# Kernel tuning notes

Hardware: AMD Instinct MI355X
Metric: run time of the kernel (lower is better)

Reference implementation:

```python
import jax, jax.numpy as jnp
import numpy as np

N = 50000        # nodes
E = 800000       # edges (no self loops; GATv2Conv adds them itself)
F_IN = 256       # n_feats
DIM_H = 64       # hidden per head (layer 1)
HEADS = 4        # heads (layer 1)
N_CLASSES = 10
NEG_SLOPE = 0.2


def setup_inputs() -> dict:
    key = jax.random.key(0)
    ks = jax.random.split(key, 12)
    x = jax.random.normal(ks[0], (N, F_IN), dtype=jnp.float32)
    # edges with src != dst so PyG's remove_self_loops is a no-op
    src = jax.random.randint(ks[1], (E,), 0, N, dtype=jnp.int32)
    off = jax.random.randint(ks[2], (E,), 1, N, dtype=jnp.int32)
    dst = (src + off) % N
    edge_index = jnp.stack([src, dst], axis=0)  # [2, E]
    HC = HEADS * DIM_H
    s1 = 1.0 / np.sqrt(F_IN)
    s2 = 1.0 / np.sqrt(HC)
    W_l1 = jax.random.normal(ks[3], (F_IN, HC), dtype=jnp.float32) * s1
    W_r1 = jax.random.normal(ks[4], (F_IN, HC), dtype=jnp.float32) * s1
    att1 = jax.random.normal(ks[5], (HEADS, DIM_H), dtype=jnp.float32) * s2
    b1 = jnp.zeros((HC,), dtype=jnp.float32)
    W_l2 = jax.random.normal(ks[6], (HC, N_CLASSES), dtype=jnp.float32) * s2
    W_r2 = jax.random.normal(ks[7], (HC, N_CLASSES), dtype=jnp.float32) * s2
    att2 = jax.random.normal(ks[8], (1, N_CLASSES), dtype=jnp.float32) * (1.0 / np.sqrt(N_CLASSES))
    b2 = jnp.zeros((N_CLASSES,), dtype=jnp.float32)
    return {"x": x, "edge_index": edge_index,
            "W_l1": W_l1, "W_r1": W_r1, "att1": att1, "b1": b1,
            "W_l2": W_l2, "W_r2": W_r2, "att2": att2, "b2": b2}


def _gatv2_layer(x, src, dst, W_l, W_r, att, b, heads, ch):
    """One GATv2Conv layer (concat heads). src/dst already include self loops."""
    n = x.shape[0]
    xl = (x @ W_l).reshape(n, heads, ch)  # source transform (messages)
    xr = (x @ W_r).reshape(n, heads, ch)  # target transform
    # per-edge GATv2 score: att . LeakyReLU(x_l[src] + x_r[dst])
    e = jax.nn.leaky_relu(xl[src] + xr[dst], NEG_SLOPE)   # [E, H, C]
    score = jnp.einsum('ehc,hc->eh', e, att)              # [E, H]
    # segment softmax over incoming edges of each dst node
    m = jax.ops.segment_max(score, dst, num_segments=n)   # [N, H]
    ex = jnp.exp(score - m[dst])
    denom = jax.ops.segment_sum(ex, dst, num_segments=n)  # [N, H]
    alpha = ex / denom[dst]                               # [E, H]
    msg = xl[src] * alpha[:, :, None]                     # [E, H, C]
    out = jax.ops.segment_sum(msg, dst, num_segments=n)   # [N, H, C]
    return out.reshape(n, heads * ch) + b


def reference(x, edge_index, W_l1, W_r1, att1, b1, W_l2, W_r2, att2, b2):
    n = x.shape[0]
    loops = jnp.arange(n, dtype=edge_index.dtype)
    src = jnp.concatenate([edge_index[0], loops])  # add_self_loops=True
    dst = jnp.concatenate([edge_index[1], loops])
    h = _gatv2_layer(x, src, dst, W_l1, W_r1, att1, b1, HEADS, DIM_H)
    h = jax.nn.relu(h)
    out = _gatv2_layer(h, src, dst, W_l2, W_r2, att2, b2, 1, N_CLASSES)
    return out
```

## Files before the change

kernel.cpp:

```cpp
#include <hip/hip_runtime.h>
#include <hip/hip_bf16.h>

typedef unsigned short u16;
typedef unsigned int u32;
typedef short bf16x8 __attribute__((ext_vector_type(8)));
typedef float f32x4 __attribute__((ext_vector_type(4)));

constexpr int N_NODES = 50000;
constexpr int N_EDGES = 800000;
constexpr int ET      = N_EDGES + N_NODES;
constexpr int HC      = 256;
constexpr int NCLS    = 10;
constexpr float NEG   = 0.2f;

__device__ __forceinline__ u16 f2bf(float f) {
  u32 u = __float_as_uint(f);
  u += 0x7fffu + ((u >> 16) & 1u);
  return (u16)(u >> 16);
}
__device__ __forceinline__ float bf2f(u16 h) {
  return __uint_as_float(((u32)h) << 16);
}

__device__ __forceinline__ float dpp_ror8(float v) {
  return __uint_as_float(__builtin_amdgcn_mov_dpp(__float_as_uint(v), 0x128, 0xf, 0xf, true));
}
__device__ __forceinline__ float dpp_ror4(float v) {
  return __uint_as_float(__builtin_amdgcn_mov_dpp(__float_as_uint(v), 0x124, 0xf, 0xf, true));
}
__device__ __forceinline__ float dpp_ror2(float v) {
  return __uint_as_float(__builtin_amdgcn_mov_dpp(__float_as_uint(v), 0x122, 0xf, 0xf, true));
}
__device__ __forceinline__ float dpp_ror1(float v) {
  return __uint_as_float(__builtin_amdgcn_mov_dpp(__float_as_uint(v), 0x121, 0xf, 0xf, true));
}
__device__ __forceinline__ float row16_allsum(float p) {
  p += dpp_ror8(p);
  p += dpp_ror4(p);
  p += dpp_ror2(p);
  p += dpp_ror1(p);
  return p;
}


__global__ void k_zero_int(int* __restrict__ p, int n) {
  int i = blockIdx.x * 256 + threadIdx.x;
  if (i < n) p[i] = 0;
}

__global__ void k_hist(const int* __restrict__ ei, int* __restrict__ counts) {
  int e = blockIdx.x * 256 + threadIdx.x;
  if (e >= ET) return;
  int d = (e < N_EDGES) ? ei[N_EDGES + e] : (e - N_EDGES);
  atomicAdd(&counts[d], 1);
}

__global__ __launch_bounds__(256) void k_scan1(const int* __restrict__ counts,
                                               int* __restrict__ offsets,
                                               int* __restrict__ bsums) {
  __shared__ int sd[256];
  int t = threadIdx.x;
  int base = blockIdx.x * 1024 + t * 4;
  int v[4];
#pragma unroll
  for (int i = 0; i < 4; ++i) {
    int idx = base + i;
    v[i] = (idx < N_NODES) ? counts[idx] : 0;
  }
  int tsum = v[0] + v[1] + v[2] + v[3];
  sd[t] = tsum;
  __syncthreads();
  for (int off = 1; off < 256; off <<= 1) {
    int x = (t >= off) ? sd[t - off] : 0;
    __syncthreads();
    sd[t] += x;
    __syncthreads();
  }
  int run = sd[t] - tsum;
#pragma unroll
  for (int i = 0; i < 4; ++i) {
    run += v[i];
    int idx = base + i;
    if (idx < N_NODES) offsets[idx + 1] = run;
  }
  if (t == 255) bsums[blockIdx.x] = sd[255];
}

__global__ __launch_bounds__(256) void k_scan2(int* __restrict__ bsums, int nb) {
  __shared__ int sd[256];
  int t = threadIdx.x;
  int v = (t < nb) ? bsums[t] : 0;
  sd[t] = v;
  __syncthreads();
  for (int off = 1; off < 256; off <<= 1) {
    int x = (t >= off) ? sd[t - off] : 0;
    __syncthreads();
    sd[t] += x;
    __syncthreads();
  }
  if (t < nb) bsums[t] = sd[t] - v;
}

__global__ void k_scan3(const int* __restrict__ bsums, int* __restrict__ offsets) {
  int i = blockIdx.x * 256 + threadIdx.x;
  if (i < N_NODES) offsets[i + 1] += bsums[i >> 10];
  if (i == 0) offsets[0] = 0;
}

__global__ void k_scatter(const int* __restrict__ ei, const int* __restrict__ offsets,
                          int* __restrict__ counts, int* __restrict__ srcs) {
  int e = blockIdx.x * 256 + threadIdx.x;
  if (e >= ET) return;
  int s, d;
  if (e < N_EDGES) { s = ei[e]; d = ei[N_EDGES + e]; }
  else             { s = e - N_EDGES; d = s; }
  int pos = offsets[d] + atomicSub(&counts[d], 1) - 1;
  srcs[pos] = s;
}

__global__ __launch_bounds__(256) void k_packW(const float* __restrict__ Wl,
                                               const float* __restrict__ Wr,
                                               u16* __restrict__ Wt_hi,
                                               u16* __restrict__ Wt_lo) {
  int c = blockIdx.x;
  int k = threadIdx.x;
  float w = (c < 256) ? Wl[k * 256 + c] : Wr[k * 256 + (c - 256)];
  u16 h = f2bf(w);
  float lo = w - bf2f(h);
  Wt_hi[c * 256 + k] = h;
  Wt_lo[c * 256 + k] = f2bf(lo);
}

__global__ __launch_bounds__(256) void k_gemm1_mfma(const float* __restrict__ x,
                                                    const u16* __restrict__ Wt_hi,
                                                    const u16* __restrict__ Wt_lo,
                                                    float* __restrict__ xl,
                                                    float* __restrict__ xr) {
  __shared__ char smem[61440];
  char* Ah = smem;
  char* Al = smem + 10240;
  char* Bh = smem + 20480;
  char* Bl = smem + 40960;

  int t = threadIdx.x;
  int lane = t & 63, wave = t >> 6;
  int wm = wave >> 1, wn = wave & 1;
  int row0 = blockIdx.x * 128;
  int bc = blockIdx.y;
  int col0 = bc * 256;

  f32x4 acc[4][8];
#pragma unroll
  for (int m = 0; m < 4; ++m)
#pragma unroll
    for (int n = 0; n < 8; ++n) acc[m][n] = (f32x4){0.f, 0.f, 0.f, 0.f};

  int ar = t >> 3;
  int ak4 = t & 7;
  int rr = lane & 15, kb = lane >> 4;

#pragma unroll 1
  for (int kk = 0; kk < 256; kk += 32) {
#pragma unroll
    for (int i = 0; i < 4; ++i) {
      int r = ar + 32 * i;
      int grow = row0 + r;
      if (grow >= N_NODES) grow = N_NODES - 1;
      float4 v = *(const float4*)&x[(size_t)grow * 256 + kk + ak4 * 4];
      u16 h0 = f2bf(v.x), h1 = f2bf(v.y), h2 = f2bf(v.z), h3 = f2bf(v.w);
      u16 l0 = f2bf(v.x - bf2f(h0)), l1 = f2bf(v.y - bf2f(h1));
      u16 l2 = f2bf(v.z - bf2f(h2)), l3 = f2bf(v.w - bf2f(h3));
      uint2 hp = make_uint2((u32)h0 | ((u32)h1 << 16), (u32)h2 | ((u32)h3 << 16));
      uint2 lp = make_uint2((u32)l0 | ((u32)l1 << 16), (u32)l2 | ((u32)l3 << 16));
      int boff = r * 80 + ak4 * 8;
      *(uint2*)(Ah + boff) = hp;
      *(uint2*)(Al + boff) = lp;
    }
    {
      const u16* sh = &Wt_hi[(size_t)(col0 + t) * 256 + kk];
      const u16* sl = &Wt_lo[(size_t)(col0 + t) * 256 + kk];
#pragma unroll
      for (int j = 0; j < 4; ++j) {
        *(uint4*)(Bh + t * 80 + j * 16) = *(const uint4*)&sh[j * 8];
        *(uint4*)(Bl + t * 80 + j * 16) = *(const uint4*)&sl[j * 8];
      }
    }
    __syncthreads();
    bf16x8 a_h[4], a_l[4];
#pragma unroll
    for (int m = 0; m < 4; ++m) {
      int off = (wm * 64 + m * 16 + rr) * 80 + kb * 16;
      a_h[m] = *(const bf16x8*)(Ah + off);
      a_l[m] = *(const bf16x8*)(Al + off);
    }
#pragma unroll
    for (int n = 0; n < 8; ++n) {
      int off = (wn * 128 + n * 16 + rr) * 80 + kb * 16;
      bf16x8 b_h = *(const bf16x8*)(Bh + off);
      bf16x8 b_l = *(const bf16x8*)(Bl + off);
#pragma unroll
      for (int m = 0; m < 4; ++m) {
        acc[m][n] = __builtin_amdgcn_mfma_f32_16x16x32_bf16(a_h[m], b_h, acc[m][n], 0, 0, 0);
        acc[m][n] = __builtin_amdgcn_mfma_f32_16x16x32_bf16(a_l[m], b_h, acc[m][n], 0, 0, 0);
        acc[m][n] = __builtin_amdgcn_mfma_f32_16x16x32_bf16(a_h[m], b_l, acc[m][n], 0, 0, 0);
      }
    }
    __syncthreads();
  }
  float* Cout = bc ? xr : xl;
  int r0w = row0 + wm * 64 + (lane >> 4) * 4;
  int c0w = wn * 128 + (lane & 15);
#pragma unroll
  for (int m = 0; m < 4; ++m)
#pragma unroll
    for (int j = 0; j < 4; ++j) {
      int grow = r0w + m * 16 + j;
      if (grow < N_NODES) {
#pragma unroll
        for (int n = 0; n < 8; ++n)
          Cout[(size_t)grow * 256 + c0w + n * 16] = acc[m][n][j];
      }
    }
}

__global__ __launch_bounds__(256) void k_gat1_fused(
    const float* __restrict__ xl, const float* __restrict__ xr,
    const float* __restrict__ att, const float* __restrict__ b1,
    const float* __restrict__ Wl2, const float* __restrict__ Wr2,
    const int* __restrict__ offsets, const int* __restrict__ srcs,
    float* __restrict__ xl2, float* __restrict__ xr2) {
  __shared__ float Ws[20][256];
  int t = threadIdx.x;
#pragma unroll
  for (int c = 0; c < 10; ++c) {
    Ws[c][t]      = Wl2[t * 10 + c];
    Ws[c + 10][t] = Wr2[t * 10 + c];
  }
  __syncthreads();

  int wave = t >> 6, lane = t & 63;
  int n = blockIdx.x * 4 + wave;
  int c0 = lane * 4;
  float4 attv = *(const float4*)&att[c0];
  float4 xrv  = *(const float4*)&xr[(size_t)n * 256 + c0];

  float m0 = -1e30f, m1 = -1e30f, m2 = -1e30f, m3 = -1e30f;
  float d0 = 0.f, d1 = 0.f, d2 = 0.f, d3 = 0.f;
  float4 A0 = {0,0,0,0}, A1 = {0,0,0,0}, A2 = {0,0,0,0}, A3 = {0,0,0,0};

  auto proc = [&](float4 xv, float& m, float& d, float4& A) {
    float e0 = xv.x + xrv.x; e0 = fmaxf(e0, NEG * e0);
    float e1 = xv.y + xrv.y; e1 = fmaxf(e1, NEG * e1);
    float e2 = xv.z + xrv.z; e2 = fmaxf(e2, NEG * e2);
    float e3 = xv.w + xrv.w; e3 = fmaxf(e3, NEG * e3);
    float p = attv.x * e0 + attv.y * e1 + attv.z * e2 + attv.w * e3;
    p = row16_allsum(p);
    float mn = fmaxf(m, p);
    float corr = __expf(m - mn);
    float w    = __expf(p - mn);
    d = d * corr + w;
    A.x = A.x * corr + w * xv.x;
    A.y = A.y * corr + w * xv.y;
    A.z = A.z * corr + w * xv.z;
    A.w = A.w * corr + w * xv.w;
    m = mn;
  };

  int jb = offsets[n], je = offsets[n + 1];
  int j = jb;
  for (; j + 4 <= je; j += 4) {
    int s0 = srcs[j], s1 = srcs[j + 1], s2 = srcs[j + 2], s3 = srcs[j + 3];
    float4 x0 = *(const float4*)&xl[(size_t)s0 * 256 + c0];
    float4 x1 = *(const float4*)&xl[(size_t)s1 * 256 + c0];
    float4 x2 = *(const float4*)&xl[(size_t)s2 * 256 + c0];
    float4 x3 = *(const float4*)&xl[(size_t)s3 * 256 + c0];
    proc(x0, m0, d0, A0);
    proc(x1, m1, d1, A1);
    proc(x2, m2, d2, A2);
    proc(x3, m3, d3, A3);
  }
  for (; j < je; ++j) {
    int s = srcs[j];
    float4 xv = *(const float4*)&xl[(size_t)s * 256 + c0];
    proc(xv, m0, d0, A0);
  }

  auto merge = [](float& ma, float& da, float4& Aa, float mb, float db, float4 Ab) {
    float mm = fmaxf(ma, mb);
    float fa = __expf(ma - mm), fb = __expf(mb - mm);
    da = da * fa + db * fb;
    Aa.x = Aa.x * fa + Ab.x * fb;
    Aa.y = Aa.y * fa + Ab.y * fb;
    Aa.z = Aa.z * fa + Ab.z * fb;
    Aa.w = Aa.w * fa + Ab.w * fb;
    ma = mm;
  };
  merge(m0, d0, A0, m1, d1, A1);
  merge(m2, d2, A2, m3, d3, A3);
  merge(m0, d0, A0, m2, d2, A2);

  float inv = 1.0f / d0;
  float4 bv = *(const float4*)&b1[c0];
  float4 ov;
  ov.x = fmaxf(A0.x * inv + bv.x, 0.f);
  ov.y = fmaxf(A0.y * inv + bv.y, 0.f);
  ov.z = fmaxf(A0.z * inv + bv.z, 0.f);
  ov.w = fmaxf(A0.w * inv + bv.w, 0.f);

  float p[20];
#pragma unroll
  for (int c = 0; c < 20; ++c) {
    float4 w4 = *(const float4*)&Ws[c][c0];
    p[c] = ov.x * w4.x + ov.y * w4.y + ov.z * w4.z + ov.w * w4.w;
  }
#pragma unroll
  for (int c = 0; c < 20; ++c) {
    p[c] = row16_allsum(p[c]);
    p[c] += __shfl_xor(p[c], 16);
    p[c] += __shfl_xor(p[c], 32);
  }
  if (lane == 0) {
#pragma unroll
    for (int c = 0; c < 10; ++c) xl2[n * NCLS + c] = p[c];
#pragma unroll
    for (int c = 0; c < 10; ++c) xr2[n * NCLS + c] = p[c + 10];
  }
}

__global__ __launch_bounds__(256) void k_gat2(const float* __restrict__ xl2,
                                              const float* __restrict__ xr2,
                                              const float* __restrict__ att2,
                                              const float* __restrict__ b2,
                                              const int* __restrict__ offsets,
                                              const int* __restrict__ srcs,
                                              float* __restrict__ out) {
  int wave = threadIdx.x >> 6;
  int lane = threadIdx.x & 63;
  int n = blockIdx.x * 4 + wave;
  if (n >= N_NODES) return;
  int g = lane >> 4;
  int k = lane & 15;
  bool act = k < NCLS;
  float attk = act ? att2[k] : 0.f;
  float xrk  = act ? xr2[n * NCLS + k] : 0.f;
  float m = -1e30f;
  float denom = 0.f, acc = 0.f;
  int jb = offsets[n], je = offsets[n + 1];
  for (int j = jb + g; j < je; j += 4) {
    int s = srcs[j];
    float xlv = act ? xl2[s * NCLS + k] : 0.f;
    float e = xlv + xrk; e = fmaxf(e, NEG * e);
    float p = attk * e;
    p = row16_allsum(p);
    float mn = fmaxf(m, p);
    float corr = __expf(m - mn);
    float w    = __expf(p - mn);
    denom = denom * corr + w;
    acc   = acc * corr + w * xlv;
    m = mn;
  }
  float mg = fmaxf(m, __shfl_xor(m, 16));
  mg = fmaxf(mg, __shfl_xor(mg, 32));
  float f = __expf(m - mg);
  float d = denom * f;
  d += __shfl_xor(d, 16);
  d += __shfl_xor(d, 32);
  float a = acc * f;
  a += __shfl_xor(a, 16);
  a += __shfl_xor(a, 32);
  if (act && g == 0) out[n * NCLS + k] = a / d + b2[k];
}


extern "C" void kernel_launch(void* const* d_in, const int* in_sizes, int n_in,
                              void* d_out, int out_size, void* d_ws, size_t ws_size,
                              hipStream_t stream) {
  const float* x    = (const float*)d_in[0];
  const int*   ei   = (const int*)d_in[1];
  const float* Wl1  = (const float*)d_in[2];
  const float* Wr1  = (const float*)d_in[3];
  const float* att1 = (const float*)d_in[4];
  const float* b1   = (const float*)d_in[5];
  const float* Wl2  = (const float*)d_in[6];
  const float* Wr2  = (const float*)d_in[7];
  const float* att2 = (const float*)d_in[8];
  const float* b2   = (const float*)d_in[9];
  float* out = (float*)d_out;

  int* offsets = (int*)d_ws;
  int* counts  = offsets + (N_NODES + 1);
  int* bsums   = counts + N_NODES;
  int* srcs    = bsums + 256;
  size_t int_count = (size_t)(N_NODES + 1) + N_NODES + 256 + ET;
  size_t foff = (int_count + 63) & ~(size_t)63;
  float* xl1 = (float*)d_ws + foff;
  float* xr1 = xl1 + (size_t)N_NODES * HC;
  u16* Wt_hi = (u16*)(xr1 + (size_t)N_NODES * HC);
  u16* Wt_lo = Wt_hi + 512 * 256;
  float* xl2 = (float*)(Wt_lo + 512 * 256);
  float* xr2 = xl2 + (size_t)N_NODES * NCLS;

  const int nthr = 256;
  k_zero_int<<<(N_NODES + nthr - 1) / nthr, nthr, 0, stream>>>(counts, N_NODES);
  k_hist<<<(ET + nthr - 1) / nthr, nthr, 0, stream>>>(ei, counts);
  int nb = (N_NODES + 1023) / 1024;
  k_scan1<<<nb, nthr, 0, stream>>>(counts, offsets, bsums);
  k_scan2<<<1, nthr, 0, stream>>>(bsums, nb);
  k_scan3<<<(N_NODES + nthr - 1) / nthr, nthr, 0, stream>>>(bsums, offsets);
  k_scatter<<<(ET + nthr - 1) / nthr, nthr, 0, stream>>>(ei, offsets, counts, srcs);

  k_packW<<<512, nthr, 0, stream>>>(Wl1, Wr1, Wt_hi, Wt_lo);
  dim3 g1((N_NODES + 127) / 128, 2);
  k_gemm1_mfma<<<g1, nthr, 0, stream>>>(x, Wt_hi, Wt_lo, xl1, xr1);

  k_gat1_fused<<<N_NODES / 4, nthr, 0, stream>>>(xl1, xr1, att1, b1, Wl2, Wr2,
                                                 offsets, srcs, xl2, xr2);

  k_gat2<<<(N_NODES + 3) / 4, nthr, 0, stream>>>(xl2, xr2, att2, b2, offsets, srcs, out);
}
```

Before: 424.0 us.

## Store layer-1 features in bf16, pad CSR rows, use lazy exp2 softmax rescaling

The GEMM now writes xl/xr as bf16 instead of fp32, which halves the bytes gathered per edge in the layer-1 aggregation. CSR segments are padded to multiples of four with -1 sentinels, so the remainder loop goes away. Online softmax now uses exp2 with log2e folded into att and skips rescaling unless the max grows by more than a threshold. The zero kernel becomes a memset. The cost is bf16 rounding error in the layer-1 features and extra memset traffic for the padded index array.

```diff
diff --git a/kernel.cpp b/kernel.cpp
--- a/kernel.cpp
+++ b/kernel.cpp
@@ -9,9 +9,11 @@
 constexpr int N_NODES = 50000;
 constexpr int N_EDGES = 800000;
 constexpr int ET      = N_EDGES + N_NODES;
+constexpr int ETP     = ET + 3 * N_NODES;
 constexpr int HC      = 256;
 constexpr int NCLS    = 10;
 constexpr float NEG   = 0.2f;
+constexpr float LOG2E = 1.442695041f;
 
 __device__ __forceinline__ u16 f2bf(float f) {
   u32 u = __float_as_uint(f);
@@ -42,11 +44,6 @@
   return p;
 }
 
-
-__global__ void k_zero_int(int* __restrict__ p, int n) {
-  int i = blockIdx.x * 256 + threadIdx.x;
-  if (i < n) p[i] = 0;
-}
 
 __global__ void k_hist(const int* __restrict__ ei, int* __restrict__ counts) {
   int e = blockIdx.x * 256 + threadIdx.x;
@@ -65,7 +62,7 @@
 #pragma unroll
   for (int i = 0; i < 4; ++i) {
     int idx = base + i;
-    v[i] = (idx < N_NODES) ? counts[idx] : 0;
+    v[i] = (idx < N_NODES) ? ((counts[idx] + 3) & ~3) : 0;
   }
   int tsum = v[0] + v[1] + v[2] + v[3];
   sd[t] = tsum;
@@ -134,8 +131,8 @@
 __global__ __launch_bounds__(256) void k_gemm1_mfma(const float* __restrict__ x,
                                                     const u16* __restrict__ Wt_hi,
                                                     const u16* __restrict__ Wt_lo,
-                                                    float* __restrict__ xl,
-                                                    float* __restrict__ xr) {
+                                                    u16* __restrict__ xlb,
+                                                    u16* __restrict__ xrb) {
   __shared__ char smem[61440];
   char* Ah = smem;
   char* Al = smem + 10240;
@@ -207,7 +204,7 @@
     }
     __syncthreads();
   }
-  float* Cout = bc ? xr : xl;
+  u16* Cout = bc ? xrb : xlb;
   int r0w = row0 + wm * 64 + (lane >> 4) * 4;
   int c0w = wn * 128 + (lane & 15);
 #pragma unroll
@@ -218,13 +215,13 @@
       if (grow < N_NODES) {
 #pragma unroll
         for (int n = 0; n < 8; ++n)
-          Cout[(size_t)grow * 256 + c0w + n * 16] = acc[m][n][j];
+          Cout[(size_t)grow * 256 + c0w + n * 16] = f2bf(acc[m][n][j]);
       }
     }
 }
 
 __global__ __launch_bounds__(256) void k_gat1_fused(
-    const float* __restrict__ xl, const float* __restrict__ xr,
+    const u16* __restrict__ xlb, const u16* __restrict__ xrb,
     const float* __restrict__ att, const float* __restrict__ b1,
     const float* __restrict__ Wl2, const float* __restrict__ Wr2,
     const int* __restrict__ offsets, const int* __restrict__ srcs,
@@ -242,52 +239,49 @@
   int n = blockIdx.x * 4 + wave;
   int c0 = lane * 4;
   float4 attv = *(const float4*)&att[c0];
-  float4 xrv  = *(const float4*)&xr[(size_t)n * 256 + c0];
+  attv.x *= LOG2E; attv.y *= LOG2E; attv.z *= LOG2E; attv.w *= LOG2E;
+  ushort4 xr4 = *(const ushort4*)&xrb[(size_t)n * 256 + c0];
+  float4 xrv = make_float4(bf2f(xr4.x), bf2f(xr4.y), bf2f(xr4.z), bf2f(xr4.w));
 
   float m0 = -1e30f, m1 = -1e30f, m2 = -1e30f, m3 = -1e30f;
   float d0 = 0.f, d1 = 0.f, d2 = 0.f, d3 = 0.f;
   float4 A0 = {0,0,0,0}, A1 = {0,0,0,0}, A2 = {0,0,0,0}, A3 = {0,0,0,0};
 
-  auto proc = [&](float4 xv, float& m, float& d, float4& A) {
+  auto proc = [&](int s, float& m, float& d, float4& A) {
+    int sa = s < 0 ? 0 : s;
+    ushort4 r4 = *(const ushort4*)&xlb[(size_t)sa * 256 + c0];
+    float4 xv = make_float4(bf2f(r4.x), bf2f(r4.y), bf2f(r4.z), bf2f(r4.w));
     float e0 = xv.x + xrv.x; e0 = fmaxf(e0, NEG * e0);
     float e1 = xv.y + xrv.y; e1 = fmaxf(e1, NEG * e1);
     float e2 = xv.z + xrv.z; e2 = fmaxf(e2, NEG * e2);
     float e3 = xv.w + xrv.w; e3 = fmaxf(e3, NEG * e3);
     float p = attv.x * e0 + attv.y * e1 + attv.z * e2 + attv.w * e3;
     p = row16_allsum(p);
-    float mn = fmaxf(m, p);
-    float corr = __expf(m - mn);
-    float w    = __expf(p - mn);
-    d = d * corr + w;
-    A.x = A.x * corr + w * xv.x;
-    A.y = A.y * corr + w * xv.y;
-    A.z = A.z * corr + w * xv.z;
-    A.w = A.w * corr + w * xv.w;
-    m = mn;
+    if (s < 0) p = -2e30f;
+    if (!__all(p <= m + 8.0f)) {
+      float mn = fmaxf(m, p);
+      float corr = exp2f(m - mn);
+      d *= corr;
+      A.x *= corr; A.y *= corr; A.z *= corr; A.w *= corr;
+      m = mn;
+    }
+    float w = exp2f(p - m);
+    d += w;
+    A.x += w * xv.x; A.y += w * xv.y; A.z += w * xv.z; A.w += w * xv.w;
   };
 
   int jb = offsets[n], je = offsets[n + 1];
-  int j = jb;
-  for (; j + 4 <= je; j += 4) {
+  for (int j = jb; j < je; j += 4) {
     int s0 = srcs[j], s1 = srcs[j + 1], s2 = srcs[j + 2], s3 = srcs[j + 3];
-    float4 x0 = *(const float4*)&xl[(size_t)s0 * 256 + c0];
-    float4 x1 = *(const float4*)&xl[(size_t)s1 * 256 + c0];
-    float4 x2 = *(const float4*)&xl[(size_t)s2 * 256 + c0];
-    float4 x3 = *(const float4*)&xl[(size_t)s3 * 256 + c0];
-    proc(x0, m0, d0, A0);
-    proc(x1, m1, d1, A1);
-    proc(x2, m2, d2, A2);
-    proc(x3, m3, d3, A3);
-  }
-  for (; j < je; ++j) {
-    int s = srcs[j];
-    float4 xv = *(const float4*)&xl[(size_t)s * 256 + c0];
-    proc(xv, m0, d0, A0);
+    proc(s0, m0, d0, A0);
+    proc(s1, m1, d1, A1);
+    proc(s2, m2, d2, A2);
+    proc(s3, m3, d3, A3);
   }
 
   auto merge = [](float& ma, float& da, float4& Aa, float mb, float db, float4 Ab) {
     float mm = fmaxf(ma, mb);
-    float fa = __expf(ma - mm), fb = __expf(mb - mm);
+    float fa = exp2f(ma - mm), fb = exp2f(mb - mm);
     da = da * fa + db * fb;
     Aa.x = Aa.x * fa + Ab.x * fb;
     Aa.y = Aa.y * fa + Ab.y * fb;
@@ -341,27 +335,32 @@
   int g = lane >> 4;
   int k = lane & 15;
   bool act = k < NCLS;
-  float attk = act ? att2[k] : 0.f;
+  float attk = act ? att2[k] * LOG2E : 0.f;
   float xrk  = act ? xr2[n * NCLS + k] : 0.f;
   float m = -1e30f;
   float denom = 0.f, acc = 0.f;
   int jb = offsets[n], je = offsets[n + 1];
   for (int j = jb + g; j < je; j += 4) {
     int s = srcs[j];
-    float xlv = act ? xl2[s * NCLS + k] : 0.f;
+    int sa = s < 0 ? 0 : s;
+    float xlv = act ? xl2[sa * NCLS + k] : 0.f;
     float e = xlv + xrk; e = fmaxf(e, NEG * e);
     float p = attk * e;
     p = row16_allsum(p);
-    float mn = fmaxf(m, p);
-    float corr = __expf(m - mn);
-    float w    = __expf(p - mn);
-    denom = denom * corr + w;
-    acc   = acc * corr + w * xlv;
-    m = mn;
+    if (s < 0) p = -2e30f;
+    if (!__all(p <= m + 8.0f)) {
+      float mn = fmaxf(m, p);
+      float corr = exp2f(m - mn);
+      denom *= corr; acc *= corr;
+      m = mn;
+    }
+    float w = exp2f(p - m);
+    denom += w;
+    acc   += w * xlv;
   }
   float mg = fmaxf(m, __shfl_xor(m, 16));
   mg = fmaxf(mg, __shfl_xor(mg, 32));
-  float f = __expf(m - mg);
+  float f = exp2f(m - mg);
   float d = denom * f;
   d += __shfl_xor(d, 16);
   d += __shfl_xor(d, 32);
@@ -391,29 +390,30 @@
   int* counts  = offsets + (N_NODES + 1);
   int* bsums   = counts + N_NODES;
   int* srcs    = bsums + 256;
-  size_t int_count = (size_t)(N_NODES + 1) + N_NODES + 256 + ET;
+  size_t int_count = (size_t)(N_NODES + 1) + N_NODES + 256 + ETP;
   size_t foff = (int_count + 63) & ~(size_t)63;
-  float* xl1 = (float*)d_ws + foff;
-  float* xr1 = xl1 + (size_t)N_NODES * HC;
-  u16* Wt_hi = (u16*)(xr1 + (size_t)N_NODES * HC);
+  u16* xlb  = (u16*)((float*)d_ws + foff);
+  u16* xrb  = xlb + (size_t)N_NODES * HC;
+  u16* Wt_hi = xrb + (size_t)N_NODES * HC;
   u16* Wt_lo = Wt_hi + 512 * 256;
   float* xl2 = (float*)(Wt_lo + 512 * 256);
   float* xr2 = xl2 + (size_t)N_NODES * NCLS;
 
   const int nthr = 256;
-  k_zero_int<<<(N_NODES + nthr - 1) / nthr, nthr, 0, stream>>>(counts, N_NODES);
+  hipMemsetAsync(counts, 0, (size_t)N_NODES * 4, stream);
   k_hist<<<(ET + nthr - 1) / nthr, nthr, 0, stream>>>(ei, counts);
   int nb = (N_NODES + 1023) / 1024;
   k_scan1<<<nb, nthr, 0, stream>>>(counts, offsets, bsums);
   k_scan2<<<1, nthr, 0, stream>>>(bsums, nb);
   k_scan3<<<(N_NODES + nthr - 1) / nthr, nthr, 0, stream>>>(bsums, offsets);
+  hipMemsetAsync(srcs, 0xFF, (size_t)ETP * 4, stream);
   k_scatter<<<(ET + nthr - 1) / nthr, nthr, 0, stream>>>(ei, offsets, counts, srcs);
 
   k_packW<<<512, nthr, 0, stream>>>(Wl1, Wr1, Wt_hi, Wt_lo);
   dim3 g1((N_NODES + 127) / 128, 2);
-  k_gemm1_mfma<<<g1, nthr, 0, stream>>>(x, Wt_hi, Wt_lo, xl1, xr1);
-
-  k_gat1_fused<<<N_NODES / 4, nthr, 0, stream>>>(xl1, xr1, att1, b1, Wl2, Wr2,
+  k_gemm1_mfma<<<g1, nthr, 0, stream>>>(x, Wt_hi, Wt_lo, xlb, xrb);
+
+  k_gat1_fused<<<N_NODES / 4, nthr, 0, stream>>>(xlb, xrb, att1, b1, Wl2, Wr2,
                                                  offsets, srcs, xl2, xr2);
 
   k_gat2<<<(N_NODES + 3) / 4, nthr, 0, stream>>>(xl2, xr2, att2, b2, offsets, srcs, out);
```

Result: slower. 432.9 us (+2.1%).
